# Kernel optimization log

Measured on AMD Instinct MI355X. Metric: run time of the kernel, lower is better.

Reference implementation:

```python
import jax, jax.numpy as jnp
import numpy as np

B, L, D = 16, 1024, 1024
H = 8
K = D // H
OUT = 64

def setup_inputs() -> dict:
    key = jax.random.key(0)
    ks = jax.random.split(key, 12)
    std = 0.1
    return {
        "x0": jax.random.normal(ks[0], (B, L, D), jnp.float32),
        "x1": jax.random.normal(ks[1], (B, L, D), jnp.float32),
        "x2": jax.random.normal(ks[2], (B, L, D), jnp.float32),
        "support": jax.random.normal(ks[3], (B, L), jnp.float32),
        "mask": jnp.ones((B, L), jnp.float32),
        "Wk": std * jax.random.normal(ks[4], (D, D), jnp.float32),   # tokeys.weight
        "Wq": std * jax.random.normal(ks[5], (D, D), jnp.float32),   # toqueries.weight
        "Wv": std * jax.random.normal(ks[6], (D, D), jnp.float32),   # tovalues.weight
        "Wu": std * jax.random.normal(ks[7], (D, D), jnp.float32),   # unifyheads.weight
        "bu": std * jax.random.normal(ks[8], (D,), jnp.float32),     # unifyheads.bias
        "Wmlp": std * jax.random.normal(ks[9], (OUT, D), jnp.float32),
        "bmlp": std * jax.random.normal(ks[10], (OUT,), jnp.float32),
    }

def reference(x0, x1, x2, support, mask, Wk, Wq, Wv, Wu, bu, Wmlp, bmlp):
    # SelfAttention with first=True: q from x2 via tokeys, k from x1 via toqueries, v from x0 via tovalues
    b, l, d = x0.shape
    h, k = H, K
    scale = k ** (-0.25)  # applied to both q and k, as in the torch code
    q = (x2 @ Wk.T).reshape(b, l, h, k) * scale
    key_ = (x1 @ Wq.T).reshape(b, l, h, k) * scale
    v = (x0 @ Wv.T).reshape(b, l, h, k)
    dot = jnp.einsum('blhk,bmhk->bhlm', q, key_)          # [b,h,l,l]
    attn = jax.nn.softmax(dot, axis=-1)
    out = jnp.einsum('bhlm,bmhk->blhk', attn, v).reshape(b, l, d)
    out = out @ Wu.T + bu                                  # unifyheads
    pooled = jnp.mean(out, axis=1) + jnp.max(out, axis=1)  # 'mean_and_max'
    logits = pooled @ Wmlp.T + bmlp                        # dropout = identity (eval)
    return logits
```

## Files before the change

kernel.cpp:

```cpp
#include <hip/hip_runtime.h>

using u16 = unsigned short;
using u32 = unsigned int;
using short8 = __attribute__((ext_vector_type(8))) short;
using floatx4 = __attribute__((ext_vector_type(4))) float;
using floatx16 = __attribute__((ext_vector_type(16))) float;

__device__ __forceinline__ u32 fbits(float f) { union { float f; u32 u; } v; v.f = f; return v.u; }
__device__ __forceinline__ float fofb(u32 u) { union { u32 u; float f; } v; v.u = u; return v.f; }

__device__ __forceinline__ u16 f2bf(float f) {
    u32 u = fbits(f);
    return (u16)((u + 0x7FFFu + ((u >> 16) & 1u)) >> 16);
}

__device__ __forceinline__ void cvt_split8(const float* x, short8& h, short8& l) {
#pragma unroll
    for (int j = 0; j < 8; ++j) {
        u32 b = fbits(x[j]);
        h[j] = (short)(b >> 16);
        float r = x[j] - fofb(b & 0xffff0000u);
        l[j] = (short)(fbits(r) >> 16);
    }
}
__device__ __forceinline__ void cvt_rne8(const float* x, short8& h) {
#pragma unroll
    for (int j = 0; j < 8; ++j) h[j] = (short)f2bf(x[j]);
}

__device__ __forceinline__ void load_lds16(const void* g, u16* l) {
    __builtin_amdgcn_global_load_lds(
        (const __attribute__((address_space(1))) unsigned int*)(g),
        (__attribute__((address_space(3))) unsigned int*)(l), 16, 0, 0);
}

__global__ void convw_kernel(const float* __restrict__ W0, const float* __restrict__ W1,
                             const float* __restrict__ W2, const float* __restrict__ W3,
                             u16* __restrict__ D0, u16* __restrict__ D1,
                             u16* __restrict__ D2, u16* __restrict__ D3) {
    int y = blockIdx.y;
    const float* s = (y == 0) ? W0 : (y == 1) ? W1 : (y == 2) ? W2 : W3;
    u16* d = (y == 0) ? D0 : (y == 1) ? D1 : (y == 2) ? D2 : D3;
    int i = (blockIdx.x * 256 + threadIdx.x) * 4;
    float4 v = *reinterpret_cast<const float4*>(s + i);
    ushort4 h;
    h.x = f2bf(v.x); h.y = f2bf(v.y); h.z = f2bf(v.z); h.w = f2bf(v.w);
    *reinterpret_cast<ushort4*>(d + i) = h;
}

#define GK 1024
#define GN 1024

template<bool SPLIT, bool TRANS, bool POOL, bool FP32A>
__global__ __launch_bounds__(256)
void gemm_bt(const void* __restrict__ Av, const u16* __restrict__ Bh,
             u16* __restrict__ Cb, float scale, u16* __restrict__ Vt,
             float* __restrict__ psum, float* __restrict__ pmax)
{
    constexpr int SM = TRANS ? 17408 : (FP32A ? 12288 : 8192);
    __shared__ __align__(16) u16 smem[SM];

    const int tid  = threadIdx.x;
    const int lane = tid & 63, wave = tid >> 6;
    const int quad = lane >> 4, l15 = lane & 15;
    const int wr = wave >> 1, wc = wave & 1;
    const int bm = blockIdx.x * 128, bn = blockIdx.y * 128;

    const int BOff = FP32A ? 8192 : 4096;

    floatx4 acc[4][4];
#pragma unroll
    for (int mt = 0; mt < 4; ++mt)
#pragma unroll
        for (int nt = 0; nt < 4; ++nt)
#pragma unroll
            for (int r = 0; r < 4; ++r) acc[mt][nt][r] = 0.f;

    const int s8 = (quad ^ ((l15 >> 1) & 3)) * 8;

    for (int kt = 0; kt < GK; kt += 32) {
        __syncthreads();
        if (FP32A) {
            const float* Af = (const float*)Av;
            const int arow = lane >> 3, achk = (lane & 7) ^ (lane >> 3);
            const int brow = lane >> 2, bchk = (lane & 3) ^ ((lane >> 3) & 3);
#pragma unroll
            for (int j = 0; j < 6; ++j) {
                int n = wave + 4 * j;
                if (n < 16) {
                    load_lds16(Af + (size_t)(bm + n * 8 + arow) * GK + kt + achk * 4,
                               smem + n * 512);
                } else {
                    int m = n - 16;
                    load_lds16(Bh + (size_t)(bn + m * 16 + brow) * GK + kt + bchk * 8,
                               smem + 8192 + m * 512);
                }
            }
        } else {
            const u16* Ab = (const u16*)Av;
            const int cgl = (lane & 3) ^ ((lane >> 3) & 3);
            const int rl  = lane >> 2;
            const u16* gp = (wave < 2) ? Ab : Bh;
            int rowb = (wave < 2) ? bm : bn;
            u16* lp = smem + (wave >> 1) * 4096;
            int q0 = (wave & 1) * 4;
#pragma unroll
            for (int q = 0; q < 4; ++q) {
                int qq = q0 + q;
                load_lds16(gp + (size_t)(rowb + qq * 16 + rl) * GK + cgl * 8 + kt,
                           lp + qq * 512);
            }
        }
        __syncthreads();

        short8 a_h[4], a_l[4], b_h[4];
        if (FP32A) {
            const float* Af4 = (const float*)smem;
#pragma unroll
            for (int mt = 0; mt < 4; ++mt) {
                int ra = wr * 64 + mt * 16 + l15;
                int f = ra & 7;
                float xv[8];
                *reinterpret_cast<float4*>(xv) =
                    *reinterpret_cast<const float4*>(Af4 + ra * 32 + (((2 * quad) ^ f) * 4));
                *reinterpret_cast<float4*>(xv + 4) =
                    *reinterpret_cast<const float4*>(Af4 + ra * 32 + (((2 * quad + 1) ^ f) * 4));
                if (SPLIT) cvt_split8(xv, a_h[mt], a_l[mt]);
                else       cvt_rne8(xv, a_h[mt]);
            }
        } else {
#pragma unroll
            for (int mt = 0; mt < 4; ++mt) {
                int ra = wr * 64 + mt * 16 + l15;
                a_h[mt] = *reinterpret_cast<const short8*>(smem + ra * 32 + s8);
            }
        }
#pragma unroll
        for (int nt = 0; nt < 4; ++nt) {
            int rb = wc * 64 + nt * 16 + l15;
            b_h[nt] = *reinterpret_cast<const short8*>(smem + BOff + rb * 32 + s8);
        }
#pragma unroll
        for (int mt = 0; mt < 4; ++mt)
#pragma unroll
            for (int nt = 0; nt < 4; ++nt)
                acc[mt][nt] = __builtin_amdgcn_mfma_f32_16x16x32_bf16(a_h[mt], b_h[nt], acc[mt][nt], 0, 0, 0);
        if (SPLIT) {
#pragma unroll
            for (int mt = 0; mt < 4; ++mt)
#pragma unroll
                for (int nt = 0; nt < 4; ++nt)
                    acc[mt][nt] = __builtin_amdgcn_mfma_f32_16x16x32_bf16(a_l[mt], b_h[nt], acc[mt][nt], 0, 0, 0);
        }
    }

    if (POOL) {
#pragma unroll
        for (int nt = 0; nt < 4; ++nt) {
            float s = 0.f, m = -3.0e38f;
#pragma unroll
            for (int mt = 0; mt < 4; ++mt)
#pragma unroll
                for (int r = 0; r < 4; ++r) {
                    float v = acc[mt][nt][r];
                    s += v; m = fmaxf(m, v);
                }
            s += __shfl_xor(s, 16); s += __shfl_xor(s, 32);
            m = fmaxf(m, __shfl_xor(m, 16)); m = fmaxf(m, __shfl_xor(m, 32));
            if (quad == 0) {
                int col = bn + wc * 64 + nt * 16 + l15;
                int chunk = (bm >> 6) + wr;
                psum[chunk * 1024 + col] = s;
                pmax[chunk * 1024 + col] = m;
            }
        }
    } else if (!TRANS) {
#pragma unroll
        for (int mt = 0; mt < 4; ++mt)
#pragma unroll
            for (int nt = 0; nt < 4; ++nt)
#pragma unroll
                for (int r = 0; r < 4; ++r) {
                    int row = bm + wr * 64 + mt * 16 + quad * 4 + r;
                    int col = bn + wc * 64 + nt * 16 + l15;
                    Cb[(size_t)row * GN + col] = f2bf(acc[mt][nt][r] * scale);
                }
    } else {
        __syncthreads();
#pragma unroll
        for (int mt = 0; mt < 4; ++mt)
#pragma unroll
            for (int nt = 0; nt < 4; ++nt)
#pragma unroll
                for (int r = 0; r < 4; ++r) {
                    int row_local = wr * 64 + mt * 16 + quad * 4 + r;
                    int col_local = wc * 64 + nt * 16 + l15;
                    smem[col_local * 136 + row_local] = f2bf(acc[mt][nt][r]);
                }
        __syncthreads();
        int b = bm >> 10, l0 = bm & 1023, h = bn >> 7;
        int d = tid >> 1, rblk = (tid & 1) * 64;
        u16* gv = Vt + ((size_t)(b * 8 + h) * 128 + d) * 1024 + l0 + rblk;
#pragma unroll
        for (int v = 0; v < 8; ++v)
            *reinterpret_cast<short8*>(gv + v * 8) =
                *reinterpret_cast<const short8*>(smem + d * 136 + rblk + v * 8);
    }
}

#define LOG2E 1.44269504088896f
#define EXPC  46.1662413084470f

__global__ __launch_bounds__(256)
void attn_kernel(const u16* __restrict__ Q, const u16* __restrict__ Kk,
                 const u16* __restrict__ Vt, u16* __restrict__ AO)
{
    __shared__ __align__(16) u16 Ks[64 * 128];
    __shared__ __align__(16) u16 Vts[128 * 64];
    __shared__ __align__(16) u16 Ps[4][32 * 64];

    const int tid  = threadIdx.x;
    const int lane = tid & 63, wave = tid >> 6;
    const int l31 = lane & 31, h2 = lane >> 5;
    const int l7 = lane & 7;
    const int qt = blockIdx.x, hd = blockIdx.y, b = blockIdx.z;

    short8 qf[8];
    {
        int qrow = b * 1024 + qt * 128 + wave * 32 + l31;
        const u16* qp = Q + (size_t)qrow * 1024 + hd * 128 + h2 * 8;
#pragma unroll
        for (int s = 0; s < 8; ++s)
            qf[s] = *reinterpret_cast<const short8*>(qp + s * 16);
    }

    float lsum = 0.f;
    floatx16 oacc[4];
#pragma unroll
    for (int db = 0; db < 4; ++db)
#pragma unroll
        for (int r = 0; r < 16; ++r) oacc[db][r] = 0.f;

    const int krow_l = lane >> 4;
    const u16* kgB[4];
#pragma unroll
    for (int i = 0; i < 4; ++i) {
        int cg = (lane & 15) ^ ((i * 4 + krow_l) & 7);
        kgB[i] = Kk + (size_t)(b * 1024 + wave * 16 + i * 4 + krow_l) * 1024
                    + hd * 128 + cg * 8;
    }
    const u16* vtb = Vt + (size_t)(b * 8 + hd) * 128 * 1024;
    const int vrow_l = lane >> 3;
    const u16* vgB = vtb + (size_t)(wave * 32 + vrow_l) * 1024
                         + (((lane & 7) ^ vrow_l) * 8);

    for (int kt2 = 0; kt2 < 16; ++kt2) {
        __syncthreads();
#pragma unroll
        for (int i = 0; i < 4; ++i)
            load_lds16(kgB[i] + (size_t)kt2 * 64 * 1024, Ks + (wave * 16 + i * 4) * 128);
#pragma unroll
        for (int i = 0; i < 4; ++i)
            load_lds16(vgB + (size_t)i * 8 * 1024 + kt2 * 64, Vts + (wave * 32 + i * 8) * 64);
        __syncthreads();

#pragma unroll
        for (int kb = 0; kb < 2; ++kb) {
            floatx16 sacc;
#pragma unroll
            for (int r = 0; r < 16; ++r) sacc[r] = 0.f;
#pragma unroll
            for (int s = 0; s < 8; ++s) {
                int key = kb * 32 + l31;
                short8 kfr = *reinterpret_cast<const short8*>(
                    &Ks[key * 128 + (((s * 2 + h2) ^ l7) * 8)]);
                sacc = __builtin_amdgcn_mfma_f32_32x32x16_bf16(kfr, qf[s], sacc, 0, 0, 0);
            }
#pragma unroll
            for (int rg = 0; rg < 4; ++rg) {
                float p0 = exp2f(fmaf(sacc[rg * 4 + 0], LOG2E, -EXPC));
                float p1 = exp2f(fmaf(sacc[rg * 4 + 1], LOG2E, -EXPC));
                float p2 = exp2f(fmaf(sacc[rg * 4 + 2], LOG2E, -EXPC));
                float p3 = exp2f(fmaf(sacc[rg * 4 + 3], LOG2E, -EXPC));
                lsum += (p0 + p1) + (p2 + p3);
                uint2 w;
                w.x = (unsigned)f2bf(p0) | ((unsigned)f2bf(p1) << 16);
                w.y = (unsigned)f2bf(p2) | ((unsigned)f2bf(p3) << 16);
                *reinterpret_cast<uint2*>(
                    &Ps[wave][l31 * 64 + ((kb * 4 + rg) ^ l7) * 8 + 4 * h2]) = w;
            }
        }

#pragma unroll
        for (int ks = 0; ks < 4; ++ks) {
            short8 pfr = *reinterpret_cast<const short8*>(
                &Ps[wave][l31 * 64 + (((ks * 2 + h2) ^ l7) * 8)]);
#pragma unroll
            for (int db = 0; db < 4; ++db) {
                int d = db * 32 + l31;
                short8 vfr = *reinterpret_cast<const short8*>(
                    &Vts[d * 64 + (((ks * 2 + h2) ^ l7) * 8)]);
                oacc[db] = __builtin_amdgcn_mfma_f32_32x32x16_bf16(pfr, vfr, oacc[db], 0, 0, 0);
            }
        }
    }

    lsum += __shfl_xor(lsum, 32);

    int qbase = b * 1024 + qt * 128 + wave * 32;
#pragma unroll
    for (int rg = 0; rg < 4; ++rg)
#pragma unroll
        for (int r = 0; r < 4; ++r) {
            int row = rg * 8 + 4 * h2 + r;
            float inv = 1.0f / __shfl(lsum, row);
            u16* ao = AO + (size_t)(qbase + row) * 1024 + hd * 128 + l31;
#pragma unroll
            for (int db = 0; db < 4; ++db)
                ao[db * 32] = f2bf(oacc[db][rg * 4 + r] * inv);
        }
}

__global__ __launch_bounds__(256)
void head_kernel(const float* __restrict__ psum, const float* __restrict__ pmax,
                 const float* __restrict__ bu, const float* __restrict__ Wmlp,
                 const float* __restrict__ bmlp, float* __restrict__ out) {
    __shared__ float pool_s[1024];
    int b = blockIdx.x, tid = threadIdx.x;
    int c4 = tid * 4;
    float4 s = {0.f, 0.f, 0.f, 0.f};
    float4 m = {-3.0e38f, -3.0e38f, -3.0e38f, -3.0e38f};
#pragma unroll
    for (int c = 0; c < 16; ++c) {
        float4 a = *reinterpret_cast<const float4*>(psum + (size_t)(b * 16 + c) * 1024 + c4);
        float4 x = *reinterpret_cast<const float4*>(pmax + (size_t)(b * 16 + c) * 1024 + c4);
        s.x += a.x; s.y += a.y; s.z += a.z; s.w += a.w;
        m.x = fmaxf(m.x, x.x); m.y = fmaxf(m.y, x.y);
        m.z = fmaxf(m.z, x.z); m.w = fmaxf(m.w, x.w);
    }
    float4 bb = *reinterpret_cast<const float4*>(bu + c4);
    pool_s[c4 + 0] = s.x * (1.0f / 1024.0f) + m.x + 2.0f * bb.x;
    pool_s[c4 + 1] = s.y * (1.0f / 1024.0f) + m.y + 2.0f * bb.y;
    pool_s[c4 + 2] = s.z * (1.0f / 1024.0f) + m.z + 2.0f * bb.z;
    pool_s[c4 + 3] = s.w * (1.0f / 1024.0f) + m.w + 2.0f * bb.w;
    __syncthreads();
    int o = tid >> 2, seg = tid & 3;
    const float4* wr = reinterpret_cast<const float4*>(Wmlp + o * 1024 + seg * 256);
    const float4* pr = reinterpret_cast<const float4*>(pool_s + seg * 256);
    float acc = 0.f;
#pragma unroll 8
    for (int i = 0; i < 64; ++i) {
        float4 a = pr[i], w = wr[i];
        acc += a.x * w.x + a.y * w.y + a.z * w.z + a.w * w.w;
    }
    acc += __shfl_xor(acc, 1);
    acc += __shfl_xor(acc, 2);
    if (seg == 0) out[b * 64 + o] = acc + bmlp[o];
}

extern "C" void kernel_launch(void* const* d_in, const int* in_sizes, int n_in,
                              void* d_out, int out_size, void* d_ws, size_t ws_size,
                              hipStream_t stream) {
    const float* x0 = (const float*)d_in[0];
    const float* x1 = (const float*)d_in[1];
    const float* x2 = (const float*)d_in[2];
    const float* Wk = (const float*)d_in[5];
    const float* Wq = (const float*)d_in[6];
    const float* Wv = (const float*)d_in[7];
    const float* Wu = (const float*)d_in[8];
    const float* bu = (const float*)d_in[9];
    const float* Wmlp = (const float*)d_in[10];
    const float* bmlp = (const float*)d_in[11];
    float* out = (float*)d_out;

    char* ws = (char*)d_ws;
    const size_t MB32 = 33554432ull;
    size_t wo = 0;
    u16* Wkh = (u16*)(ws + wo); wo += 2097152;
    u16* Wqh = (u16*)(ws + wo); wo += 2097152;
    u16* Wvh = (u16*)(ws + wo); wo += 2097152;
    u16* Wuh = (u16*)(ws + wo); wo += 2097152;
    u16* Qb = (u16*)(ws + wo); wo += MB32;
    u16* Kb = (u16*)(ws + wo); wo += MB32;
    u16* Vt = (u16*)(ws + wo); wo += MB32;
    u16* AOb = (u16*)(ws + wo); wo += MB32;
    float* psum = (float*)(ws + wo); wo += 1048576;
    float* pmax = (float*)(ws + wo); wo += 1048576;
    if (ws_size < wo) return;

    const float scale = 0.29730177875068026f;

    convw_kernel<<<dim3(1024, 4), 256, 0, stream>>>(Wk, Wq, Wv, Wu, Wkh, Wqh, Wvh, Wuh);

    dim3 ggrid(128, 8);
    gemm_bt<true, false, false, true><<<ggrid, 256, 0, stream>>>(x2, Wkh, Qb, scale, nullptr, nullptr, nullptr);
    gemm_bt<true, false, false, true><<<ggrid, 256, 0, stream>>>(x1, Wqh, Kb, scale, nullptr, nullptr, nullptr);
    gemm_bt<false, true, false, true><<<ggrid, 256, 0, stream>>>(x0, Wvh, nullptr, 1.0f, Vt, nullptr, nullptr);

    dim3 agrid(8, 8, 16);
    attn_kernel<<<agrid, 256, 0, stream>>>(Qb, Kb, Vt, AOb);

    gemm_bt<false, false, true, false><<<ggrid, 256, 0, stream>>>(AOb, Wuh, nullptr, 1.0f, nullptr, psum, pmax);

    head_kernel<<<16, 256, 0, stream>>>(psum, pmax, bu, Wmlp, bmlp, out);
}
```

Before: 614.5 us.

## Double-buffer K/V tiles, keep P in registers via permlane swaps

The attention kernel now double-buffers the K and V LDS tiles, so the next tile's global-to-LDS load is issued before computing on the current one, with a single barrier per iteration. The softmax probabilities are no longer written to and read back from LDS. They are packed with v_cvt_pk_bf16_f32 and rearranged across half-waves with permlane32_swap to form the PV MFMA operand directly. It also raises wave priority around the MFMA blocks, sets launch bounds to 2 blocks per CU, and remaps block indices so blocks sharing a batch and head are scheduled together. The LDS footprint grows, and the register reshuffle must match the MFMA operand layout exactly.

```diff
diff --git a/kernel.cpp b/kernel.cpp
--- a/kernel.cpp
+++ b/kernel.cpp
@@ -5,6 +5,7 @@
 using short8 = __attribute__((ext_vector_type(8))) short;
 using floatx4 = __attribute__((ext_vector_type(4))) float;
 using floatx16 = __attribute__((ext_vector_type(16))) float;
+using u32x4 = __attribute__((ext_vector_type(4))) u32;
 
 __device__ __forceinline__ u32 fbits(float f) { union { float f; u32 u; } v; v.f = f; return v.u; }
 __device__ __forceinline__ float fofb(u32 u) { union { u32 u; float f; } v; v.u = u; return v.f; }
@@ -12,6 +13,12 @@
 __device__ __forceinline__ u16 f2bf(float f) {
     u32 u = fbits(f);
     return (u16)((u + 0x7FFFu + ((u >> 16) & 1u)) >> 16);
+}
+
+__device__ __forceinline__ u32 cvtpk_bf16(float lo, float hi) {
+    u32 r;
+    asm("v_cvt_pk_bf16_f32 %0, %1, %2" : "=v"(r) : "v"(lo), "v"(hi));
+    return r;
 }
 
 __device__ __forceinline__ void cvt_split8(const float* x, short8& h, short8& l) {
@@ -211,19 +218,22 @@
 #define LOG2E 1.44269504088896f
 #define EXPC  46.1662413084470f
 
-__global__ __launch_bounds__(256)
+__global__ __launch_bounds__(256, 2)
 void attn_kernel(const u16* __restrict__ Q, const u16* __restrict__ Kk,
                  const u16* __restrict__ Vt, u16* __restrict__ AO)
 {
-    __shared__ __align__(16) u16 Ks[64 * 128];
-    __shared__ __align__(16) u16 Vts[128 * 64];
-    __shared__ __align__(16) u16 Ps[4][32 * 64];
+    __shared__ __align__(16) u16 Ks[2][64 * 128];
+    __shared__ __align__(16) u16 Vts[2][128 * 64];
 
     const int tid  = threadIdx.x;
     const int lane = tid & 63, wave = tid >> 6;
     const int l31 = lane & 31, h2 = lane >> 5;
     const int l7 = lane & 7;
-    const int qt = blockIdx.x, hd = blockIdx.y, b = blockIdx.z;
+
+    const int lin = blockIdx.x + (blockIdx.y << 3) + (blockIdx.z << 6);
+    const int qt = lin >> 7;
+    const int hd = lin & 7;
+    const int b  = (lin >> 3) & 15;
 
     short8 qf[8];
     {
@@ -254,55 +264,85 @@
     const u16* vgB = vtb + (size_t)(wave * 32 + vrow_l) * 1024
                          + (((lane & 7) ^ vrow_l) * 8);
 
-    for (int kt2 = 0; kt2 < 16; ++kt2) {
-        __syncthreads();
-#pragma unroll
-        for (int i = 0; i < 4; ++i)
-            load_lds16(kgB[i] + (size_t)kt2 * 64 * 1024, Ks + (wave * 16 + i * 4) * 128);
-#pragma unroll
-        for (int i = 0; i < 4; ++i)
-            load_lds16(vgB + (size_t)i * 8 * 1024 + kt2 * 64, Vts + (wave * 32 + i * 8) * 64);
-        __syncthreads();
-
+#pragma unroll
+    for (int i = 0; i < 4; ++i)
+        load_lds16(kgB[i], &Ks[0][(wave * 16 + i * 4) * 128]);
+#pragma unroll
+    for (int i = 0; i < 4; ++i)
+        load_lds16(vgB + (size_t)i * 8 * 1024, &Vts[0][(wave * 32 + i * 8) * 64]);
+
+    for (int t = 0; t < 16; ++t) {
+        const int cur = t & 1;
+        asm volatile("s_waitcnt vmcnt(0)" ::: "memory");
+        __builtin_amdgcn_s_barrier();
+        __builtin_amdgcn_sched_barrier(0);
+        if (t < 15) {
+            const int nxt = cur ^ 1;
+#pragma unroll
+            for (int i = 0; i < 4; ++i)
+                load_lds16(kgB[i] + (size_t)(t + 1) * 64 * 1024,
+                           &Ks[nxt][(wave * 16 + i * 4) * 128]);
+#pragma unroll
+            for (int i = 0; i < 4; ++i)
+                load_lds16(vgB + (size_t)i * 8 * 1024 + (size_t)(t + 1) * 64,
+                           &Vts[nxt][(wave * 32 + i * 8) * 64]);
+        }
+        const u16* ksb = Ks[cur];
+        const u16* vsb = Vts[cur];
+
+        short8 pfr[4];
 #pragma unroll
         for (int kb = 0; kb < 2; ++kb) {
             floatx16 sacc;
 #pragma unroll
             for (int r = 0; r < 16; ++r) sacc[r] = 0.f;
+            __builtin_amdgcn_s_setprio(1);
 #pragma unroll
             for (int s = 0; s < 8; ++s) {
-                int key = kb * 32 + l31;
                 short8 kfr = *reinterpret_cast<const short8*>(
-                    &Ks[key * 128 + (((s * 2 + h2) ^ l7) * 8)]);
+                    &ksb[(kb * 32 + l31) * 128 + (((s * 2 + h2) ^ l7) * 8)]);
                 sacc = __builtin_amdgcn_mfma_f32_32x32x16_bf16(kfr, qf[s], sacc, 0, 0, 0);
             }
-#pragma unroll
-            for (int rg = 0; rg < 4; ++rg) {
-                float p0 = exp2f(fmaf(sacc[rg * 4 + 0], LOG2E, -EXPC));
-                float p1 = exp2f(fmaf(sacc[rg * 4 + 1], LOG2E, -EXPC));
-                float p2 = exp2f(fmaf(sacc[rg * 4 + 2], LOG2E, -EXPC));
-                float p3 = exp2f(fmaf(sacc[rg * 4 + 3], LOG2E, -EXPC));
-                lsum += (p0 + p1) + (p2 + p3);
-                uint2 w;
-                w.x = (unsigned)f2bf(p0) | ((unsigned)f2bf(p1) << 16);
-                w.y = (unsigned)f2bf(p2) | ((unsigned)f2bf(p3) << 16);
-                *reinterpret_cast<uint2*>(
-                    &Ps[wave][l31 * 64 + ((kb * 4 + rg) ^ l7) * 8 + 4 * h2]) = w;
-            }
-        }
-
+            __builtin_amdgcn_s_setprio(0);
+#pragma unroll
+            for (int r = 0; r < 16; ++r) {
+                float p = exp2f(fmaf(sacc[r], LOG2E, -EXPC));
+                sacc[r] = p;
+                lsum += p;
+            }
+            u32 c0[4], c1[4];
+#pragma unroll
+            for (int qd = 0; qd < 4; ++qd) {
+                c0[qd] = cvtpk_bf16(sacc[4 * qd + 0], sacc[4 * qd + 1]);
+                c1[qd] = cvtpk_bf16(sacc[4 * qd + 2], sacc[4 * qd + 3]);
+            }
+#pragma unroll
+            for (int pb = 0; pb < 2; ++pb) {
+                auto r1a = __builtin_amdgcn_permlane32_swap(c0[2 * pb],     c1[2 * pb],     false, false);
+                auto r2a = __builtin_amdgcn_permlane32_swap(c1[2 * pb],     c0[2 * pb],     false, false);
+                auto r1b = __builtin_amdgcn_permlane32_swap(c0[2 * pb + 1], c1[2 * pb + 1], false, false);
+                auto r2b = __builtin_amdgcn_permlane32_swap(c1[2 * pb + 1], c0[2 * pb + 1], false, false);
+                u32 w0 = h2 ? (u32)r2b[0] : (u32)r1a[0];
+                u32 w1 = h2 ? (u32)r1b[0] : (u32)r2a[0];
+                u32 w2 = h2 ? (u32)r2b[1] : (u32)r1a[1];
+                u32 w3 = h2 ? (u32)r1b[1] : (u32)r2a[1];
+                u32x4 ww = {w0, w1, w2, w3};
+                pfr[kb * 2 + pb] = __builtin_bit_cast(short8, ww);
+            }
+        }
+
+        __builtin_amdgcn_s_setprio(1);
 #pragma unroll
         for (int ks = 0; ks < 4; ++ks) {
-            short8 pfr = *reinterpret_cast<const short8*>(
-                &Ps[wave][l31 * 64 + (((ks * 2 + h2) ^ l7) * 8)]);
 #pragma unroll
             for (int db = 0; db < 4; ++db) {
                 int d = db * 32 + l31;
                 short8 vfr = *reinterpret_cast<const short8*>(
-                    &Vts[d * 64 + (((ks * 2 + h2) ^ l7) * 8)]);
-                oacc[db] = __builtin_amdgcn_mfma_f32_32x32x16_bf16(pfr, vfr, oacc[db], 0, 0, 0);
-            }
-        }
+                    &vsb[d * 64 + (((ks * 2 + h2) ^ l7) * 8)]);
+                oacc[db] = __builtin_amdgcn_mfma_f32_32x32x16_bf16(pfr[ks], vfr, oacc[db], 0, 0, 0);
+            }
+        }
+        __builtin_amdgcn_s_setprio(0);
     }
 
     lsum += __shfl_xor(lsum, 32);
```

Result: faster. 596.4 us (-2.9%).
